# Performance work log

Measured on AMD Instinct MI355X. Metric: run time of the kernel, lower is better.

Reference implementation:

```python
import jax, jax.numpy as jnp
import numpy as np

K = 3        # kernel_size
UM = 2       # um_dim
EPS = 1e-6
SLOPE = 0.01 # F.leaky_relu default negative slope


def setup_inputs() -> dict:
    key = jax.random.key(0)
    k1, k2, k3 = jax.random.split(key, 3)
    B, C, H, Wd = 16, 64, 64, 64
    O = 64
    xx = jax.random.normal(k1, (B, C, H, Wd), dtype=jnp.float32)
    W = jax.random.normal(k2, (O, C, K, K), dtype=jnp.float32) * 0.05
    b = jax.random.normal(k3, (O,), dtype=jnp.float32) * 0.05
    return {"xx": xx, "W": W, "b": b}


def reference(xx, W, b):
    B, C, H, Wd = xx.shape
    O = W.shape[0]
    p = (K - 1) // 2
    # replicate pad (mode='replicate' in torch == 'edge' in numpy/jax)
    xp = jnp.pad(xx, ((0, 0), (0, 0), (p, p), (p, p)), mode='edge')
    # unfold -> patches[b, c, i, j, h, w] = xp[b, c, h+i, w+j]; stride==1
    pats = jnp.stack(
        [xp[:, :, i:i + H, j:j + Wd] for i in range(K) for j in range(K)],
        axis=2,
    ).reshape(B, C, K, K, H, Wd)
    # min-max "std" normalization over (channel-group, ki, kj)
    g = pats.reshape(B, C // UM, UM, K, K, H, Wd)
    stds = (g.max(axis=(1, 3, 4), keepdims=True)
            - g.min(axis=(1, 3, 4), keepdims=True))  # [B,1,UM,1,1,H,W]
    normed = (g / (stds + EPS)).reshape(B, C, K, K, H, Wd)
    # patch-conv with stride=k on the unfolded image is equivalent to this
    # per-position contraction; big[b,c,h*k+j, w*k+i] = normed[b,c,i,j,h,w]
    # so the kernel indexes as W[o, c, j, i].
    out = jnp.einsum('bcijhw,ocji->bohw', normed, W) + b[None, :, None, None]
    out = jnp.where(out >= 0, out, SLOPE * out)  # leaky_relu
    # inverse transform: re-scale by (stds + eps)
    stds_s = stds.reshape(B, 1, UM, H, Wd)
    out = out.reshape(B, O // UM, UM, H, Wd) * (stds_s + EPS)
    return out.reshape(B, O, H, Wd)
```

## Files before the change

kernel.cpp:

```cpp
#include <hip/hip_runtime.h>
#include <hip/hip_bf16.h>

#define B_  16
#define C_  64
#define H_  64
#define W_  64
#define O_  64
#define EPS 1e-6f
#define SLOPE 0.01f

typedef __bf16  bf16x8 __attribute__((ext_vector_type(8)));
typedef float   f32x4  __attribute__((ext_vector_type(4)));

#define XT_OFF   0
#define XT_SZ    36864
#define PMIN_OFF 36864
#define PMAX_OFF 38912
#define SINV_OFF 40960
#define SEPS_OFF 42000
#undef  SEPS_OFF
#define SEPS_OFF 41984
#define SMEM_SZ  43008

__device__ __forceinline__ unsigned short f2bf(float f) {
  unsigned u = __float_as_uint(f);
  u += 0x7fffu + ((u >> 16) & 1u);
  return (unsigned short)(u >> 16);
}

__device__ __forceinline__ int clampi(int v, int lo, int hi) {
  return v < lo ? lo : (v > hi ? hi : v);
}

__global__ void wtransform_kernel(const float* __restrict__ Wsrc,
                                  unsigned short* __restrict__ Wt) {
  int idx = blockIdx.x * 256 + threadIdx.x;
  if (idx >= O_ * C_ * 9) return;
  int i = idx % 3;
  int j = (idx / 3) % 3;
  int c = (idx / 9) % C_;
  int o = idx / (9 * C_);
  int tap = i * 3 + j;
  Wt[((tap * 2 + (c & 1)) * 64 + o) * 32 + (c >> 1)] = f2bf(Wsrc[idx]);
}

__launch_bounds__(256, 3)
__global__ void conv_main_kernel(const float* __restrict__ x,
                                 const unsigned short* __restrict__ Wt,
                                 const float* __restrict__ bias,
                                 float* __restrict__ out) {
  __shared__ char smem[SMEM_SZ];
  const int tid  = threadIdx.x;
  const int lane = tid & 63;
  const int wv   = tid >> 6;
  const int b    = blockIdx.x >> 5;
  const int h0   = (blockIdx.x & 31) << 1;

  {
    const int w = tid & 63;
    const int r = tid >> 6;
    const int hr = clampi(h0 - 1 + r, 0, H_ - 1);
    const float* xb = x + ((size_t)b * C_ * H_ * W_) + hr * W_ + w;
    float mn[2] = {3.4e38f, 3.4e38f}, mx[2] = {-3.4e38f, -3.4e38f};
    #pragma unroll
    for (int pm = 0; pm < 8; ++pm) {
      const int p = pm >> 2, m = pm & 3;
      unsigned d[4];
      #pragma unroll
      for (int e = 0; e < 4; ++e) {
        const int c2a = m * 8 + 2 * e;
        const float f0 = xb[(2 * c2a + p) * (H_ * W_)];
        const float f1 = xb[(2 * (c2a + 1) + p) * (H_ * W_)];
        mn[p] = fminf(mn[p], fminf(f0, f1));
        mx[p] = fmaxf(mx[p], fmaxf(f0, f1));
        d[e] = (unsigned)f2bf(f0) | ((unsigned)f2bf(f1) << 16);
      }
      *(uint4*)(smem + XT_OFF + (r * 64 + w) * 144 + p * 64 + m * 16) =
          make_uint4(d[0], d[1], d[2], d[3]);
    }
    ((float*)(smem + PMIN_OFF))[(0 * 4 + r) * 64 + w] = mn[0];
    ((float*)(smem + PMIN_OFF))[(1 * 4 + r) * 64 + w] = mn[1];
    ((float*)(smem + PMAX_OFF))[(0 * 4 + r) * 64 + w] = mx[0];
    ((float*)(smem + PMAX_OFF))[(1 * 4 + r) * 64 + w] = mx[1];
  }
  __syncthreads();

  {
    const int hh = tid >> 7, p = (tid >> 6) & 1, w = tid & 63;
    const float* pmin = (const float*)(smem + PMIN_OFF);
    const float* pmax = (const float*)(smem + PMAX_OFF);
    float mn = 3.4e38f, mx = -3.4e38f;
    #pragma unroll
    for (int r = 0; r < 3; ++r) {
      #pragma unroll
      for (int dw = -1; dw <= 1; ++dw) {
        const int wc = clampi(w + dw, 0, W_ - 1);
        mn = fminf(mn, pmin[(p * 4 + (hh + r)) * 64 + wc]);
        mx = fmaxf(mx, pmax[(p * 4 + (hh + r)) * 64 + wc]);
      }
    }
    const float sv = (mx - mn) + EPS;
    ((float*)(smem + SEPS_OFF))[(hh * 2 + p) * 64 + w] = sv;
    ((float*)(smem + SINV_OFF))[(hh * 2 + p) * 64 + w] = 1.0f / sv;
  }
  __syncthreads();

  const int o0  = wv * 16;
  const int l15 = lane & 15;
  const int q   = lane >> 4;

  const f32x4 zero = {0.0f, 0.0f, 0.0f, 0.0f};
  f32x4 acc[2][2][4];
  #pragma unroll
  for (int p = 0; p < 2; ++p)
    #pragma unroll
    for (int hh = 0; hh < 2; ++hh)
      #pragma unroll
      for (int nt = 0; nt < 4; ++nt) acc[p][hh][nt] = zero;

  #pragma unroll
  for (int p = 0; p < 2; ++p) {
    bf16x8 af[9];
    #pragma unroll
    for (int t9 = 0; t9 < 9; ++t9)
      af[t9] = *(const bf16x8*)(Wt + ((t9 * 2 + p) * 64 + o0 + l15) * 32 + q * 8);
    #pragma unroll
    for (int xr = 0; xr < 4; ++xr) {
      #pragma unroll
      for (int nt = 0; nt < 4; ++nt) {
        bf16x8 bfr[3];
        #pragma unroll
        for (int j = 0; j < 3; ++j) {
          const int wc = clampi(nt * 16 + l15 + j - 1, 0, W_ - 1);
          bfr[j] = *(const bf16x8*)(smem + XT_OFF + (xr * 64 + wc) * 144 + p * 64 + q * 16);
        }
        #pragma unroll
        for (int hh = 0; hh < 2; ++hh) {
          const int i = xr - hh;
          if (i >= 0 && i < 3) {
            #pragma unroll
            for (int j = 0; j < 3; ++j)
              acc[p][hh][nt] = __builtin_amdgcn_mfma_f32_16x16x32_bf16(
                  af[i * 3 + j], bfr[j], acc[p][hh][nt], 0, 0, 0);
          }
        }
      }
    }
  }

  const float* sinv = (const float*)(smem + SINV_OFF);
  const float* seps = (const float*)(smem + SEPS_OFF);
  #pragma unroll
  for (int hh = 0; hh < 2; ++hh) {
    #pragma unroll
    for (int nt = 0; nt < 4; ++nt) {
      const int wpx = nt * 16 + l15;
      const float s0 = sinv[(hh * 2 + 0) * 64 + wpx];
      const float s1 = sinv[(hh * 2 + 1) * 64 + wpx];
      const float se0 = seps[(hh * 2 + 0) * 64 + wpx];
      const float se1 = seps[(hh * 2 + 1) * 64 + wpx];
      #pragma unroll
      for (int reg = 0; reg < 4; ++reg) {
        const int o = o0 + q * 4 + reg;
        float v = acc[0][hh][nt][reg] * s0 + acc[1][hh][nt][reg] * s1 + bias[o];
        v = v >= 0.0f ? v : SLOPE * v;
        v *= (o & 1) ? se1 : se0;
        out[((b * O_ + o) * H_ + (h0 + hh)) * W_ + wpx] = v;
      }
    }
  }
}

extern "C" void kernel_launch(void* const* d_in, const int* in_sizes, int n_in,
                              void* d_out, int out_size, void* d_ws, size_t ws_size,
                              hipStream_t stream) {
  const float* x    = (const float*)d_in[0];
  const float* Wsrc = (const float*)d_in[1];
  const float* bias = (const float*)d_in[2];
  float* out = (float*)d_out;
  unsigned short* Wt = (unsigned short*)d_ws;

  wtransform_kernel<<<144, 256, 0, stream>>>(Wsrc, Wt);
  conv_main_kernel<<<512, 256, 0, stream>>>(x, Wt, bias, out);
}
```

Measured before the change: 82.44 us.

## Split conv into prep pass writing bf16 planes and per-row MFMA kernel

The fused kernel is split into two. A prep kernel converts x to packed bf16 planes in workspace and stores per-row channel min/max. A gemm kernel then handles one output row per block, reading the halo rows straight from global memory and computing the stds with wave shuffles instead of LDS. This removes the redundant halo loads and the LDS staging of the old 2-row tiles and doubles the grid size. In exchange it adds an extra global round trip for the bf16 tensor and the min/max maps, plus one more kernel launch.

Result: slower. 92.82 us (+12.6%).

```diff
diff --git a/kernel.cpp b/kernel.cpp
--- a/kernel.cpp
+++ b/kernel.cpp
@@ -12,15 +12,8 @@
 typedef __bf16  bf16x8 __attribute__((ext_vector_type(8)));
 typedef float   f32x4  __attribute__((ext_vector_type(4)));
 
-#define XT_OFF   0
-#define XT_SZ    36864
-#define PMIN_OFF 36864
-#define PMAX_OFF 38912
-#define SINV_OFF 40960
-#define SEPS_OFF 42000
-#undef  SEPS_OFF
-#define SEPS_OFF 41984
-#define SMEM_SZ  43008
+#define XT_WS_OFF  131072
+#define PMM_WS_OFF 16908288
 
 __device__ __forceinline__ unsigned short f2bf(float f) {
   unsigned u = __float_as_uint(f);
@@ -44,129 +37,154 @@
   Wt[((tap * 2 + (c & 1)) * 64 + o) * 32 + (c >> 1)] = f2bf(Wsrc[idx]);
 }
 
-__launch_bounds__(256, 3)
-__global__ void conv_main_kernel(const float* __restrict__ x,
-                                 const unsigned short* __restrict__ Wt,
-                                 const float* __restrict__ bias,
-                                 float* __restrict__ out) {
-  __shared__ char smem[SMEM_SZ];
-  const int tid  = threadIdx.x;
-  const int lane = tid & 63;
-  const int wv   = tid >> 6;
-  const int b    = blockIdx.x >> 5;
-  const int h0   = (blockIdx.x & 31) << 1;
-
-  {
-    const int w = tid & 63;
-    const int r = tid >> 6;
-    const int hr = clampi(h0 - 1 + r, 0, H_ - 1);
-    const float* xb = x + ((size_t)b * C_ * H_ * W_) + hr * W_ + w;
-    float mn[2] = {3.4e38f, 3.4e38f}, mx[2] = {-3.4e38f, -3.4e38f};
-    #pragma unroll
-    for (int pm = 0; pm < 8; ++pm) {
-      const int p = pm >> 2, m = pm & 3;
-      unsigned d[4];
-      #pragma unroll
-      for (int e = 0; e < 4; ++e) {
-        const int c2a = m * 8 + 2 * e;
-        const float f0 = xb[(2 * c2a + p) * (H_ * W_)];
-        const float f1 = xb[(2 * (c2a + 1) + p) * (H_ * W_)];
-        mn[p] = fminf(mn[p], fminf(f0, f1));
-        mx[p] = fmaxf(mx[p], fmaxf(f0, f1));
-        d[e] = (unsigned)f2bf(f0) | ((unsigned)f2bf(f1) << 16);
-      }
-      *(uint4*)(smem + XT_OFF + (r * 64 + w) * 144 + p * 64 + m * 16) =
-          make_uint4(d[0], d[1], d[2], d[3]);
-    }
-    ((float*)(smem + PMIN_OFF))[(0 * 4 + r) * 64 + w] = mn[0];
-    ((float*)(smem + PMIN_OFF))[(1 * 4 + r) * 64 + w] = mn[1];
-    ((float*)(smem + PMAX_OFF))[(0 * 4 + r) * 64 + w] = mx[0];
-    ((float*)(smem + PMAX_OFF))[(1 * 4 + r) * 64 + w] = mx[1];
-  }
+__global__ __launch_bounds__(256)
+void prep_kernel(const float* __restrict__ x,
+                 char* __restrict__ xt,
+                 float* __restrict__ pmm) {
+  __shared__ float red[2][2][4][64];
+  const int bb = blockIdx.x;
+  const int b  = bb >> 6;
+  const int h  = bb & 63;
+  const int qq = threadIdx.x >> 6;
+  const int w  = threadIdx.x & 63;
+
+  const float* xp = x + (((size_t)b * C_ + qq * 16) * H_ + h) * W_ + w;
+  float f[16];
+  #pragma unroll
+  for (int k = 0; k < 16; ++k) f[k] = xp[(size_t)k * (H_ * W_)];
+
+  float mn[2] = {3.4e38f, 3.4e38f}, mx[2] = {-3.4e38f, -3.4e38f};
+  unsigned pk[2][4];
+  #pragma unroll
+  for (int k = 0; k < 16; ++k) {
+    const int p = k & 1, e = k >> 1;
+    mn[p] = fminf(mn[p], f[k]);
+    mx[p] = fmaxf(mx[p], f[k]);
+    const unsigned h16 = f2bf(f[k]);
+    if (e & 1) pk[p][e >> 1] |= (h16 << 16);
+    else       pk[p][e >> 1]  = h16;
+  }
+  #pragma unroll
+  for (int p = 0; p < 2; ++p)
+    *(uint4*)(xt + ((size_t)(((b * 2 + p) * 4 + qq) * 4096) + h * 64 + w) * 16) =
+        make_uint4(pk[p][0], pk[p][1], pk[p][2], pk[p][3]);
+
+  red[0][0][qq][w] = mn[0];
+  red[0][1][qq][w] = mn[1];
+  red[1][0][qq][w] = mx[0];
+  red[1][1][qq][w] = mx[1];
   __syncthreads();
 
-  {
-    const int hh = tid >> 7, p = (tid >> 6) & 1, w = tid & 63;
-    const float* pmin = (const float*)(smem + PMIN_OFF);
-    const float* pmax = (const float*)(smem + PMAX_OFF);
+  const int map = threadIdx.x >> 7;
+  const int p   = (threadIdx.x >> 6) & 1;
+  const int w2  = threadIdx.x & 63;
+  float v;
+  if (map == 0)
+    v = fminf(fminf(red[0][p][0][w2], red[0][p][1][w2]),
+              fminf(red[0][p][2][w2], red[0][p][3][w2]));
+  else
+    v = fmaxf(fmaxf(red[1][p][0][w2], red[1][p][1][w2]),
+              fmaxf(red[1][p][2][w2], red[1][p][3][w2]));
+  pmm[((size_t)(map * 16 + b) * 2 + p) * 4096 + h * 64 + w2] = v;
+}
+
+__global__ __launch_bounds__(256, 4)
+void gemm_kernel(const char* __restrict__ xt,
+                 const unsigned short* __restrict__ Wt,
+                 const float* __restrict__ pmm,
+                 const float* __restrict__ bias,
+                 float* __restrict__ out) {
+  const int bb   = blockIdx.x;
+  const int b    = bb >> 6;
+  const int h    = bb & 63;
+  const int wv   = threadIdx.x >> 6;
+  const int lane = threadIdx.x & 63;
+  const int l15  = lane & 15;
+  const int q    = lane >> 4;
+  const int o0   = wv * 16;
+
+  float si[2], se[2];
+  #pragma unroll
+  for (int p = 0; p < 2; ++p) {
     float mn = 3.4e38f, mx = -3.4e38f;
     #pragma unroll
     for (int r = 0; r < 3; ++r) {
-      #pragma unroll
-      for (int dw = -1; dw <= 1; ++dw) {
-        const int wc = clampi(w + dw, 0, W_ - 1);
-        mn = fminf(mn, pmin[(p * 4 + (hh + r)) * 64 + wc]);
-        mx = fmaxf(mx, pmax[(p * 4 + (hh + r)) * 64 + wc]);
-      }
-    }
+      const int hr = clampi(h - 1 + r, 0, H_ - 1);
+      mn = fminf(mn, pmm[((size_t)(0 * 16 + b) * 2 + p) * 4096 + hr * 64 + lane]);
+      mx = fmaxf(mx, pmm[((size_t)(1 * 16 + b) * 2 + p) * 4096 + hr * 64 + lane]);
+    }
+    const float mnl = __shfl(mn, clampi(lane - 1, 0, 63));
+    const float mnr = __shfl(mn, clampi(lane + 1, 0, 63));
+    const float mxl = __shfl(mx, clampi(lane - 1, 0, 63));
+    const float mxr = __shfl(mx, clampi(lane + 1, 0, 63));
+    mn = fminf(mn, fminf(mnl, mnr));
+    mx = fmaxf(mx, fmaxf(mxl, mxr));
     const float sv = (mx - mn) + EPS;
-    ((float*)(smem + SEPS_OFF))[(hh * 2 + p) * 64 + w] = sv;
-    ((float*)(smem + SINV_OFF))[(hh * 2 + p) * 64 + w] = 1.0f / sv;
-  }
-  __syncthreads();
-
-  const int o0  = wv * 16;
-  const int l15 = lane & 15;
-  const int q   = lane >> 4;
+    se[p] = sv;
+    si[p] = 1.0f / sv;
+  }
 
   const f32x4 zero = {0.0f, 0.0f, 0.0f, 0.0f};
-  f32x4 acc[2][2][4];
-  #pragma unroll
-  for (int p = 0; p < 2; ++p)
-    #pragma unroll
-    for (int hh = 0; hh < 2; ++hh)
-      #pragma unroll
-      for (int nt = 0; nt < 4; ++nt) acc[p][hh][nt] = zero;
-
-  #pragma unroll
+  f32x4 oacc[4];
+  #pragma unroll
+  for (int nt = 0; nt < 4; ++nt) oacc[nt] = zero;
+
+  #pragma unroll 1
   for (int p = 0; p < 2; ++p) {
     bf16x8 af[9];
     #pragma unroll
     for (int t9 = 0; t9 < 9; ++t9)
       af[t9] = *(const bf16x8*)(Wt + ((t9 * 2 + p) * 64 + o0 + l15) * 32 + q * 8);
-    #pragma unroll
-    for (int xr = 0; xr < 4; ++xr) {
+
+    const char* plane = xt + (size_t)(((b * 2 + p) * 4 + q) * 4096) * 16;
+    f32x4 acc[4];
+    #pragma unroll
+    for (int nt = 0; nt < 4; ++nt) acc[nt] = zero;
+
+    #pragma unroll
+    for (int i = 0; i < 3; ++i) {
+      const int hr = clampi(h - 1 + i, 0, H_ - 1);
+      const char* row = plane + (size_t)hr * 64 * 16;
       #pragma unroll
       for (int nt = 0; nt < 4; ++nt) {
         bf16x8 bfr[3];
         #pragma unroll
         for (int j = 0; j < 3; ++j) {
           const int wc = clampi(nt * 16 + l15 + j - 1, 0, W_ - 1);
-          bfr[j] = *(const bf16x8*)(smem + XT_OFF + (xr * 64 + wc) * 144 + p * 64 + q * 16);
+          bfr[j] = *(const bf16x8*)(row + wc * 16);
         }
         #pragma unroll
-        for (int hh = 0; hh < 2; ++hh) {
-          const int i = xr - hh;
-          if (i >= 0 && i < 3) {
-            #pragma unroll
-            for (int j = 0; j < 3; ++j)
-              acc[p][hh][nt] = __builtin_amdgcn_mfma_f32_16x16x32_bf16(
-                  af[i * 3 + j], bfr[j], acc[p][hh][nt], 0, 0, 0);
-          }
-        }
+        for (int j = 0; j < 3; ++j)
+          acc[nt] = __builtin_amdgcn_mfma_f32_16x16x32_bf16(
+              af[i * 3 + j], bfr[j], acc[nt], 0, 0, 0);
       }
     }
-  }
-
-  const float* sinv = (const float*)(smem + SINV_OFF);
-  const float* seps = (const float*)(smem + SEPS_OFF);
-  #pragma unroll
-  for (int hh = 0; hh < 2; ++hh) {
+
     #pragma unroll
     for (int nt = 0; nt < 4; ++nt) {
-      const int wpx = nt * 16 + l15;
-      const float s0 = sinv[(hh * 2 + 0) * 64 + wpx];
-      const float s1 = sinv[(hh * 2 + 1) * 64 + wpx];
-      const float se0 = seps[(hh * 2 + 0) * 64 + wpx];
-      const float se1 = seps[(hh * 2 + 1) * 64 + wpx];
+      const float sv = __shfl(si[p], nt * 16 + l15);
       #pragma unroll
-      for (int reg = 0; reg < 4; ++reg) {
-        const int o = o0 + q * 4 + reg;
-        float v = acc[0][hh][nt][reg] * s0 + acc[1][hh][nt][reg] * s1 + bias[o];
-        v = v >= 0.0f ? v : SLOPE * v;
-        v *= (o & 1) ? se1 : se0;
-        out[((b * O_ + o) * H_ + (h0 + hh)) * W_ + wpx] = v;
-      }
+      for (int reg = 0; reg < 4; ++reg)
+        oacc[nt][reg] += acc[nt][reg] * sv;
+    }
+  }
+
+  float bv[4];
+  #pragma unroll
+  for (int reg = 0; reg < 4; ++reg) bv[reg] = bias[o0 + q * 4 + reg];
+
+  #pragma unroll
+  for (int nt = 0; nt < 4; ++nt) {
+    const int wpx = nt * 16 + l15;
+    const float se0 = __shfl(se[0], wpx);
+    const float se1 = __shfl(se[1], wpx);
+    #pragma unroll
+    for (int reg = 0; reg < 4; ++reg) {
+      const int o = o0 + q * 4 + reg;
+      float v = oacc[nt][reg] + bv[reg];
+      v = v >= 0.0f ? v : SLOPE * v;
+      v *= (reg & 1) ? se1 : se0;
+      out[(((size_t)b * O_ + o) * H_ + h) * W_ + wpx] = v;
     }
   }
 }
@@ -178,8 +196,12 @@
   const float* Wsrc = (const float*)d_in[1];
   const float* bias = (const float*)d_in[2];
   float* out = (float*)d_out;
+
   unsigned short* Wt = (unsigned short*)d_ws;
+  char*  xt  = (char*)d_ws + XT_WS_OFF;
+  float* pmm = (float*)((char*)d_ws + PMM_WS_OFF);
 
   wtransform_kernel<<<144, 256, 0, stream>>>(Wsrc, Wt);
-  conv_main_kernel<<<512, 256, 0, stream>>>(x, Wt, bias, out);
-}
+  prep_kernel<<<1024, 256, 0, stream>>>(x, xt, pmm);
+  gemm_kernel<<<1024, 256, 0, stream>>>(xt, Wt, pmm, bias, out);
+}
```
